# Kernel tuning notes

Measured on AMD Instinct MI355X. Metric: run time of the kernel, lower is better.

Reference implementation:

```python
import jax, jax.numpy as jnp
import numpy as np

B, M, N_CTR, K = 16, 2048, 512, 32
DIM, DEPTH, HEADS = 384, 6, 6
EMB = 48  # fourier embedding dim (48//6 = 8 freqs per axis, basis [3,24])


def make_basis():
    e = (2.0 ** np.arange(EMB // 6)).astype(np.float32) * np.pi  # [8]
    z = np.zeros(EMB // 6, np.float32)
    basis = np.stack([np.concatenate([e, z, z]),
                      np.concatenate([z, e, z]),
                      np.concatenate([z, z, e])])  # [3, 24]
    return jnp.asarray(basis)


def fourier_embed(x, basis):
    # x [..., 3] -> [..., 48]  (sin/cos of 24 frequency projections)
    p = jnp.einsum('...d,de->...e', x, basis)
    return jnp.concatenate([jnp.sin(p), jnp.cos(p)], axis=-1)


def fps_idx(pos, n):
    # farthest point sampling, deterministic start at index 0. pos [M,3] -> [n]
    d0 = jnp.sum((pos - pos[0]) ** 2, -1)
    def step(d, _):
        i = jnp.argmax(d)
        d = jnp.minimum(d, jnp.sum((pos - pos[i]) ** 2, -1))
        return d, i
    _, idxs = jax.lax.scan(step, d0, None, length=n - 1)
    return jnp.concatenate([jnp.zeros(1, jnp.int32), idxs.astype(jnp.int32)])


def layernorm(x, g, b, eps=1e-6):
    m = jnp.mean(x, -1, keepdims=True)
    v = jnp.var(x, -1, keepdims=True)
    return (x - m) * jax.lax.rsqrt(v + eps) * g + b


def _lin(key, fi, fo):
    kw, kb = jax.random.split(key)
    w = jax.random.normal(kw, (fi, fo), jnp.float32) / np.sqrt(fi)
    b = jax.random.normal(kb, (fo,), jnp.float32) * 0.01
    return w, b


def setup_inputs() -> dict:
    key = jax.random.key(0)
    ks = jax.random.split(key, 16)
    pc = jax.random.uniform(ks[0], (B, M, 3), jnp.float32)
    embed_w, embed_b = _lin(ks[1], 3 + EMB, DIM)
    lw1, lb1 = _lin(ks[2], 3 + EMB, 256)
    lw2, lb2 = _lin(ks[3], 256, 256)
    gw1, gb1 = _lin(ks[4], 256, 256)
    gw2, gb2 = _lin(ks[5], 256, DIM)
    def stack_lin(k, fi, fo):
        kk = jax.random.split(k, DEPTH)
        ws, bs = zip(*[_lin(kk[i], fi, fo) for i in range(DEPTH)])
        return jnp.stack(ws), jnp.stack(bs)
    qkv_w, qkv_b = stack_lin(ks[6], DIM, 3 * DIM)
    proj_w, proj_b = stack_lin(ks[7], DIM, DIM)
    fc1_w, fc1_b = stack_lin(ks[8], DIM, 4 * DIM)
    fc2_w, fc2_b = stack_lin(ks[9], 4 * DIM, DIM)
    return dict(
        pc=pc, embed_w=embed_w, embed_b=embed_b,
        lw1=lw1, lb1=lb1, lw2=lw2, lb2=lb2,
        gw1=gw1, gb1=gb1, gw2=gw2, gb2=gb2,
        ln1_g=jnp.ones((DEPTH, DIM)), ln1_b=jnp.zeros((DEPTH, DIM)),
        qkv_w=qkv_w, qkv_b=qkv_b, proj_w=proj_w, proj_b=proj_b,
        gamma1=jax.random.normal(ks[10], (DEPTH, DIM)) * 0.1,
        ln2_g=jnp.ones((DEPTH, DIM)), ln2_b=jnp.zeros((DEPTH, DIM)),
        fc1_w=fc1_w, fc1_b=fc1_b, fc2_w=fc2_w, fc2_b=fc2_b,
        gamma2=jax.random.normal(ks[11], (DEPTH, DIM)) * 0.1,
        lnf_g=jnp.ones((DIM,)), lnf_b=jnp.zeros((DIM,)),
    )


def reference(pc, embed_w, embed_b, lw1, lb1, lw2, lb2, gw1, gb1, gw2, gb2,
              ln1_g, ln1_b, qkv_w, qkv_b, proj_w, proj_b, gamma1,
              ln2_g, ln2_b, fc1_w, fc1_b, fc2_w, fc2_b, gamma2, lnf_g, lnf_b):
    basis = make_basis()
    # --- FPS centers (per batch) ---
    idx = jax.vmap(lambda p: fps_idx(p, N_CTR))(pc)                 # [B,N]
    centers = jnp.take_along_axis(pc, idx[:, :, None], axis=1)      # [B,N,3]
    # --- KNN graph: for each center, K nearest of the M points ---
    d2 = jnp.sum((centers[:, :, None, :] - pc[:, None, :, :]) ** 2, -1)  # [B,N,M]
    _, nn_idx = jax.lax.top_k(-d2, K)                               # [B,N,K]
    # --- PointConv: gather -> local MLP -> max-scatter -> global MLP ---
    src = jax.vmap(lambda p, i: p[i])(pc, nn_idx)                   # [B,N,K,3]
    rel = src - centers[:, :, None, :]
    feat = jnp.concatenate([rel, fourier_embed(rel, basis)], -1)    # [B,N,K,51]
    h = jax.nn.relu(feat @ lw1 + lb1) @ lw2 + lb2                   # [B,N,K,256]
    h = jnp.max(h, axis=2)  # scatter_max over edges == max over K neighbors
    x = jax.nn.relu(h @ gw1 + gb1) @ gw2 + gb2                      # [B,N,DIM]
    # --- positional embedding tokens ---
    pe = jnp.concatenate([centers, fourier_embed(centers, basis)], -1) @ embed_w + embed_b
    x = x + pe
    # --- ViT blocks (pre-LN, LayerScale, eval mode: no dropout/droppath) ---
    hd = DIM // HEADS
    scale = hd ** -0.5
    for l in range(DEPTH):
        xn = layernorm(x, ln1_g[l], ln1_b[l])
        qkv = (xn @ qkv_w[l] + qkv_b[l]).reshape(B, N_CTR, 3, HEADS, hd)
        q, k, v = jnp.moveaxis(qkv, 2, 0)                           # [B,N,H,hd]
        att = jax.nn.softmax(jnp.einsum('bqhd,bkhd->bhqk', q, k) * scale, axis=-1)
        o = jnp.einsum('bhqk,bkhd->bqhd', att, v).reshape(B, N_CTR, DIM)
        x = x + gamma1[l] * (o @ proj_w[l] + proj_b[l])
        xn = layernorm(x, ln2_g[l], ln2_b[l])
        mlp = jax.nn.gelu(xn @ fc1_w[l] + fc1_b[l], approximate=False) @ fc2_w[l] + fc2_b[l]
        x = x + gamma2[l] * mlp
    out = layernorm(x, lnf_g, lnf_b)
    return out, centers
```

## Files before the change

kernel.cpp:

```cpp
#include <hip/hip_runtime.h>
#include <math.h>

#define NB 16
#define NM 2048
#define NCTR 512
#define NK 32
#define NDIM 384

typedef unsigned long long ull;
typedef unsigned int uint;
typedef unsigned short ushort;
typedef __attribute__((ext_vector_type(8))) short bf16x8;
typedef __attribute__((ext_vector_type(4))) float f32x4;

__device__ __forceinline__ float dist2_exact(float ax, float ay, float az,
                                             float bx, float by, float bz) {
  float dx = __fsub_rn(ax, bx);
  float dy = __fsub_rn(ay, by);
  float dz = __fsub_rn(az, bz);
  return __fadd_rn(__fadd_rn(__fmul_rn(dx, dx), __fmul_rn(dy, dy)),
                   __fmul_rn(dz, dz));
}

__device__ __forceinline__ float gelu_f(float x) {
  return 0.5f * x * (1.0f + erff(x * 0.70710678118654752f));
}

__device__ __forceinline__ ushort f2bf(float f) {
  uint u = __float_as_uint(f);
  return (ushort)((u + 0x7FFFu + ((u >> 16) & 1u)) >> 16);
}
__device__ __forceinline__ float bf2f(ushort h) {
  return __uint_as_float(((uint)h) << 16);
}

__device__ __forceinline__ void cvt8(float4 p, float4 q, uint4& hi, uint4& lo) {
  float v0 = p.x, v1 = p.y, v2 = p.z, v3 = p.w;
  float v4 = q.x, v5 = q.y, v6 = q.z, v7 = q.w;
  ushort h0 = f2bf(v0), h1 = f2bf(v1), h2 = f2bf(v2), h3 = f2bf(v3);
  ushort h4 = f2bf(v4), h5 = f2bf(v5), h6 = f2bf(v6), h7 = f2bf(v7);
  ushort l0 = f2bf(v0 - bf2f(h0)), l1 = f2bf(v1 - bf2f(h1));
  ushort l2 = f2bf(v2 - bf2f(h2)), l3 = f2bf(v3 - bf2f(h3));
  ushort l4 = f2bf(v4 - bf2f(h4)), l5 = f2bf(v5 - bf2f(h5));
  ushort l6 = f2bf(v6 - bf2f(h6)), l7 = f2bf(v7 - bf2f(h7));
  hi.x = (uint)h0 | ((uint)h1 << 16); hi.y = (uint)h2 | ((uint)h3 << 16);
  hi.z = (uint)h4 | ((uint)h5 << 16); hi.w = (uint)h6 | ((uint)h7 << 16);
  lo.x = (uint)l0 | ((uint)l1 << 16); lo.y = (uint)l2 | ((uint)l3 << 16);
  lo.z = (uint)l4 | ((uint)l5 << 16); lo.w = (uint)l6 | ((uint)l7 << 16);
}

__device__ __forceinline__ void split_store(float v, ushort* H, ushort* L,
                                            size_t off) {
  ushort hi = f2bf(v);
  H[off] = hi;
  L[off] = f2bf(v - bf2f(hi));
}

__global__ __launch_bounds__(256)
void fps_kernel(const float* __restrict__ pc, float* __restrict__ centers) {
  int b = blockIdx.x;
  __shared__ float4 pos4[NM];
  __shared__ ull red[2][4];
  const float* pb = pc + (size_t)b * (NM * 3);
  int tid = threadIdx.x, lane = tid & 63, wv = tid >> 6;
  float px[8], py[8], pz[8];
#pragma unroll
  for (int i = 0; i < 8; ++i) {
    int p = tid + 256 * i;
    float x = pb[3 * p], y = pb[3 * p + 1], z = pb[3 * p + 2];
    px[i] = x; py[i] = y; pz[i] = z;
    pos4[p] = make_float4(x, y, z, 0.f);
  }
  __syncthreads();
  float* cb = centers + (size_t)b * (NCTR * 3);
  float4 s0 = pos4[0];
  float sx = s0.x, sy = s0.y, sz = s0.z;
  if (tid == 0) { cb[0] = sx; cb[1] = sy; cb[2] = sz; }
  float d[8];
  for (int n = 1; n < NCTR; ++n) {
    ull best = 0;
#pragma unroll
    for (int i = 0; i < 8; ++i) {
      int p = tid + 256 * i;
      float nd = dist2_exact(px[i], py[i], pz[i], sx, sy, sz);
      d[i] = (n == 1) ? nd : fminf(d[i], nd);
      ull key = ((ull)__float_as_uint(d[i]) << 32) | (unsigned)(0x7FFFFFFF - p);
      best = best > key ? best : key;
    }
#pragma unroll
    for (int off = 32; off; off >>= 1) {
      ull o = __shfl_xor(best, off);
      best = best > o ? best : o;
    }
    if (lane == 0) red[n & 1][wv] = best;
    __syncthreads();
    ull g0 = red[n & 1][0], g1 = red[n & 1][1];
    ull g2 = red[n & 1][2], g3 = red[n & 1][3];
    ull ga = g0 > g1 ? g0 : g1;
    ull gc2 = g2 > g3 ? g2 : g3;
    ull gb = ga > gc2 ? ga : gc2;
    int j = 0x7FFFFFFF - (int)(unsigned)(gb & 0xFFFFFFFFull);
    float4 np = pos4[j];
    sx = np.x; sy = np.y; sz = np.z;
    if (tid == 0) { cb[n * 3] = sx; cb[n * 3 + 1] = sy; cb[n * 3 + 2] = sz; }
  }
}

__global__ __launch_bounds__(256, 2)
void knn_kernel(const float* __restrict__ pc, const float* __restrict__ centers,
                int* __restrict__ nn) {
  __shared__ float pos[NM * 3];
  int b = blockIdx.x >> 7;
  int n0 = (blockIdx.x & 127) << 2;
  const float* pb = pc + (size_t)b * (NM * 3);
  for (int i = threadIdx.x; i < NM * 3; i += 256) pos[i] = pb[i];
  __syncthreads();
  int wv = threadIdx.x >> 6, lane = threadIdx.x & 63;
  int gc = b * NCTR + n0 + wv;
  float cx = centers[gc * 3], cy = centers[gc * 3 + 1], cz = centers[gc * 3 + 2];
  ull key[32];
  ull gmin[4];
#pragma unroll
  for (int g = 0; g < 4; ++g) {
    gmin[g] = ~0ull;
#pragma unroll
    for (int i = 0; i < 8; ++i) {
      int r = g * 8 + i;
      int p = lane + (r << 6);
      float nd = dist2_exact(pos[3 * p], pos[3 * p + 1], pos[3 * p + 2], cx, cy, cz);
      key[r] = ((ull)__float_as_uint(nd) << 11) | (unsigned)p;
      gmin[g] = gmin[g] < key[r] ? gmin[g] : key[r];
    }
  }
  ull a01 = gmin[0] < gmin[1] ? gmin[0] : gmin[1];
  ull a23 = gmin[2] < gmin[3] ? gmin[2] : gmin[3];
  ull lmin = a01 < a23 ? a01 : a23;
  int* nnc = nn + (size_t)gc * NK;
  for (int round = 0; round < NK; ++round) {
    ull w = lmin;
#pragma unroll
    for (int off = 32; off; off >>= 1) {
      ull o = __shfl_xor(w, off);
      w = w < o ? w : o;
    }
    if (lmin == w) {
      nnc[round] = (int)(w & 2047ull);
#pragma unroll
      for (int g = 0; g < 4; ++g) {
        if (gmin[g] == w) {
          gmin[g] = ~0ull;
#pragma unroll
          for (int i = 0; i < 8; ++i) {
            int r = g * 8 + i;
            key[r] = (key[r] == w) ? ~0ull : key[r];
            gmin[g] = gmin[g] < key[r] ? gmin[g] : key[r];
          }
        }
      }
      ull b01 = gmin[0] < gmin[1] ? gmin[0] : gmin[1];
      ull b23 = gmin[2] < gmin[3] ? gmin[2] : gmin[3];
      lmin = b01 < b23 ? b01 : b23;
    }
  }
}

__global__ __launch_bounds__(256)
void wconv(const float* __restrict__ W, ushort* __restrict__ out, int K8, int N,
           int Ksrc) {
  int c = blockIdx.x * 256 + threadIdx.x;
  if (c >= K8 * N) return;
  int kb = c / N, n = c - kb * N;
  float v[8];
#pragma unroll
  for (int i = 0; i < 8; ++i) {
    int row = kb * 8 + i;
    v[i] = (row < Ksrc) ? W[(size_t)row * N + n] : 0.f;
  }
  float4 p, q;
  p.x = v[0]; p.y = v[1]; p.z = v[2]; p.w = v[3];
  q.x = v[4]; q.y = v[5]; q.z = v[6]; q.w = v[7];
  uint4 hi, lo;
  cvt8(p, q, hi, lo);
  *(uint4*)(out + (size_t)c * 8) = hi;
  *(uint4*)(out + (size_t)(K8 * N + c) * 8) = lo;
}

__global__ __launch_bounds__(256, 2)
void edge_mfma(const float* __restrict__ pc, const float* __restrict__ centers,
               const int* __restrict__ nn, const ushort* __restrict__ lw1s,
               const float* __restrict__ lb1, const ushort* __restrict__ lw2s,
               const float* __restrict__ lb2, ushort* __restrict__ hH,
               ushort* __restrict__ hL) {
  __shared__ __align__(16) ushort featH[4096], featL[4096];
  __shared__ __align__(16) ushort t1H[16384], t1L[16384];
  int tid = threadIdx.x;
  int w = tid >> 6, lane = tid & 63;
  int l15 = lane & 15, l4 = lane >> 4;
  int wbase = w << 6;
  {
    int e = tid >> 2, s = tid & 3;
    int ge = blockIdx.x * 64 + e;
    int c = ge >> 5;
    int b = c >> 9;
    int j = nn[ge];
    const float* sp = pc + ((size_t)b * NM + j) * 3;
    float rx = sp[0] - centers[c * 3];
    float ry = sp[1] - centers[c * 3 + 1];
    float rz = sp[2] - centers[c * 3 + 2];
    auto putk = [&](int k, float v) {
      ushort hi = f2bf(v);
      ushort lo = f2bf(v - bf2f(hi));
      int idx = ((k >> 3) * 64 + e) * 8 + (k & 7);
      featH[idx] = hi;
      featL[idx] = lo;
    };
    if (s < 3) {
      float r = (s == 0) ? rx : (s == 1) ? ry : rz;
#pragma unroll
      for (int f = 0; f < 8; ++f) {
        float ef = (float)(M_PI * (double)(1 << f));
        float p = r * ef;
        putk(3 + 8 * s + f, sinf(p));
        putk(27 + 8 * s + f, cosf(p));
      }
    } else {
      putk(0, rx);
      putk(1, ry);
      putk(2, rz);
#pragma unroll
      for (int k = 51; k < 64; ++k) putk(k, 0.f);
    }
  }
  __syncthreads();
  const ushort* lw1H = lw1s;
  const ushort* lw1L = lw1s + 8 * 256 * 8;
  f32x4 acc1[4][4];
#pragma unroll
  for (int i = 0; i < 4; ++i)
#pragma unroll
    for (int j = 0; j < 4; ++j) acc1[i][j] = (f32x4){0.f, 0.f, 0.f, 0.f};
#pragma unroll
  for (int ks = 0; ks < 2; ++ks) {
    bf16x8 ah[4], al[4];
#pragma unroll
    for (int fm = 0; fm < 4; ++fm) {
      int idx = ((ks * 4 + l4) * 64 + fm * 16 + l15) * 8;
      ah[fm] = *(const bf16x8*)&featH[idx];
      al[fm] = *(const bf16x8*)&featL[idx];
    }
#pragma unroll
    for (int fn = 0; fn < 4; ++fn) {
      int col = wbase + fn * 16 + l15;
      size_t boff = ((size_t)(ks * 4 + l4) * 256 + col) * 8;
      bf16x8 bh = *(const bf16x8*)(lw1H + boff);
      bf16x8 bl = *(const bf16x8*)(lw1L + boff);
#pragma unroll
      for (int fm = 0; fm < 4; ++fm) {
        acc1[fm][fn] = __builtin_amdgcn_mfma_f32_16x16x32_bf16(al[fm], bh, acc1[fm][fn], 0, 0, 0);
        acc1[fm][fn] = __builtin_amdgcn_mfma_f32_16x16x32_bf16(ah[fm], bl, acc1[fm][fn], 0, 0, 0);
        acc1[fm][fn] = __builtin_amdgcn_mfma_f32_16x16x32_bf16(ah[fm], bh, acc1[fm][fn], 0, 0, 0);
      }
    }
  }
#pragma unroll
  for (int fn = 0; fn < 4; ++fn) {
    int chan = wbase + fn * 16 + l15;
    float bias = lb1[chan];
    int kb = chan >> 3, k7 = chan & 7;
#pragma unroll
    for (int fm = 0; fm < 4; ++fm) {
#pragma unroll
      for (int r = 0; r < 4; ++r) {
        int edge = fm * 16 + l4 * 4 + r;
        float v = fmaxf(acc1[fm][fn][r] + bias, 0.f);
        ushort hi = f2bf(v);
        ushort lo = f2bf(v - bf2f(hi));
        int idx = (kb * 64 + edge) * 8 + k7;
        t1H[idx] = hi;
        t1L[idx] = lo;
      }
    }
  }
  __syncthreads();
  const ushort* lw2H = lw2s;
  const ushort* lw2L = lw2s + 32 * 256 * 8;
  f32x4 acc2[4][4];
#pragma unroll
  for (int i = 0; i < 4; ++i)
#pragma unroll
    for (int j = 0; j < 4; ++j) acc2[i][j] = (f32x4){0.f, 0.f, 0.f, 0.f};
#pragma unroll
  for (int ks = 0; ks < 8; ++ks) {
    bf16x8 ah[4], al[4];
#pragma unroll
    for (int fm = 0; fm < 4; ++fm) {
      int idx = ((ks * 4 + l4) * 64 + fm * 16 + l15) * 8;
      ah[fm] = *(const bf16x8*)&t1H[idx];
      al[fm] = *(const bf16x8*)&t1L[idx];
    }
#pragma unroll
    for (int fn = 0; fn < 4; ++fn) {
      int col = wbase + fn * 16 + l15;
      size_t boff = ((size_t)(ks * 4 + l4) * 256 + col) * 8;
      bf16x8 bh = *(const bf16x8*)(lw2H + boff);
      bf16x8 bl = *(const bf16x8*)(lw2L + boff);
#pragma unroll
      for (int fm = 0; fm < 4; ++fm) {
        acc2[fm][fn] = __builtin_amdgcn_mfma_f32_16x16x32_bf16(al[fm], bh, acc2[fm][fn], 0, 0, 0);
        acc2[fm][fn] = __builtin_amdgcn_mfma_f32_16x16x32_bf16(ah[fm], bl, acc2[fm][fn], 0, 0, 0);
        acc2[fm][fn] = __builtin_amdgcn_mfma_f32_16x16x32_bf16(ah[fm], bh, acc2[fm][fn], 0, 0, 0);
      }
    }
  }
#pragma unroll
  for (int fn = 0; fn < 4; ++fn) {
    int col = wbase + fn * 16 + l15;
    float m0 = -INFINITY, m1 = -INFINITY;
#pragma unroll
    for (int r = 0; r < 4; ++r) {
      m0 = fmaxf(m0, fmaxf(acc2[0][fn][r], acc2[1][fn][r]));
      m1 = fmaxf(m1, fmaxf(acc2[2][fn][r], acc2[3][fn][r]));
    }
    m0 = fmaxf(m0, __shfl_xor(m0, 16));
    m0 = fmaxf(m0, __shfl_xor(m0, 32));
    m1 = fmaxf(m1, __shfl_xor(m1, 16));
    m1 = fmaxf(m1, __shfl_xor(m1, 32));
    if (l4 == 0) {
      float bias = lb2[col];
      int c0 = blockIdx.x * 2;
      split_store(m0 + bias, hH, hL, (size_t)c0 * 256 + col);
      split_store(m1 + bias, hH, hL, (size_t)(c0 + 1) * 256 + col);
    }
  }
}

template <int EPI, int OUTS>
__global__ __launch_bounds__(256, 2)
void gemm_s(const ushort* __restrict__ AH, const ushort* __restrict__ AL,
            const ushort* __restrict__ Wh, const ushort* __restrict__ Wl,
            const float* __restrict__ bias, const float* __restrict__ gamma,
            const float* __restrict__ resid, float* __restrict__ C,
            ushort* __restrict__ CH, ushort* __restrict__ CL,
            int M, int N, int K) {
  __shared__ __align__(16) ushort Ah[4096], Al[4096], Bh[4096], Bl[4096];
  int tid = threadIdx.x;
  int bn = blockIdx.x << 7, bm = blockIdx.y << 7;
  int wid = tid >> 6, lane = tid & 63;
  int wr = wid >> 1, wc = wid & 1;
  int l15 = lane & 15, l4 = lane >> 4;

  int arow = tid >> 1, akb0 = (tid & 1) << 1;
  const ushort* ApH = AH + (size_t)(bm + arow) * K + (akb0 << 3);
  const ushort* ApL = AL + (size_t)(bm + arow) * K + (akb0 << 3);
  int wkb = tid >> 7, wn = tid & 127;

  f32x4 acc[4][4];
#pragma unroll
  for (int i = 0; i < 4; ++i)
#pragma unroll
    for (int j = 0; j < 4; ++j) acc[i][j] = (f32x4){0.f, 0.f, 0.f, 0.f};

  uint4 a0 = *(const uint4*)(ApH + 0);
  uint4 a1 = *(const uint4*)(ApH + 8);
  uint4 a2 = *(const uint4*)(ApL + 0);
  uint4 a3 = *(const uint4*)(ApL + 8);
  size_t wo1 = ((size_t)wkb * N + bn + wn) * 8;
  size_t wo2 = ((size_t)(wkb + 2) * N + bn + wn) * 8;
  uint4 w0 = *(const uint4*)(Wh + wo1);
  uint4 w1 = *(const uint4*)(Wh + wo2);
  uint4 w2 = *(const uint4*)(Wl + wo1);
  uint4 w3 = *(const uint4*)(Wl + wo2);

  int nkt = K >> 5;
  for (int kt = 0; kt < nkt; ++kt) {
    *(uint4*)&Ah[(akb0 * 128 + arow) * 8] = a0;
    *(uint4*)&Ah[((akb0 + 1) * 128 + arow) * 8] = a1;
    *(uint4*)&Al[(akb0 * 128 + arow) * 8] = a2;
    *(uint4*)&Al[((akb0 + 1) * 128 + arow) * 8] = a3;
    *(uint4*)&Bh[tid * 8] = w0;
    *(uint4*)&Bh[(tid + 256) * 8] = w1;
    *(uint4*)&Bl[tid * 8] = w2;
    *(uint4*)&Bl[(tid + 256) * 8] = w3;
    __syncthreads();
    if (kt + 1 < nkt) {
      a0 = *(const uint4*)(ApH + (kt + 1) * 32 + 0);
      a1 = *(const uint4*)(ApH + (kt + 1) * 32 + 8);
      a2 = *(const uint4*)(ApL + (kt + 1) * 32 + 0);
      a3 = *(const uint4*)(ApL + (kt + 1) * 32 + 8);
      size_t b1 = ((size_t)((kt + 1) * 4 + wkb) * N + bn + wn) * 8;
      size_t b2 = ((size_t)((kt + 1) * 4 + wkb + 2) * N + bn + wn) * 8;
      w0 = *(const uint4*)(Wh + b1);
      w1 = *(const uint4*)(Wh + b2);
      w2 = *(const uint4*)(Wl + b1);
      w3 = *(const uint4*)(Wl + b2);
    }
    bf16x8 ahf[4], alf[4];
#pragma unroll
    for (int fm = 0; fm < 4; ++fm) {
      int ci = l4 * 128 + wr * 64 + fm * 16 + l15;
      ahf[fm] = *(bf16x8*)&Ah[ci * 8];
      alf[fm] = *(bf16x8*)&Al[ci * 8];
    }
#pragma unroll
    for (int fn = 0; fn < 4; ++fn) {
      int ci = l4 * 128 + wc * 64 + fn * 16 + l15;
      bf16x8 bh = *(bf16x8*)&Bh[ci * 8];
      bf16x8 bl = *(bf16x8*)&Bl[ci * 8];
#pragma unroll
      for (int fm = 0; fm < 4; ++fm) {
        acc[fm][fn] = __builtin_amdgcn_mfma_f32_16x16x32_bf16(alf[fm], bh, acc[fm][fn], 0, 0, 0);
        acc[fm][fn] = __builtin_amdgcn_mfma_f32_16x16x32_bf16(ahf[fm], bl, acc[fm][fn], 0, 0, 0);
        acc[fm][fn] = __builtin_amdgcn_mfma_f32_16x16x32_bf16(ahf[fm], bh, acc[fm][fn], 0, 0, 0);
      }
    }
    __syncthreads();
  }

#pragma unroll
  for (int fn = 0; fn < 4; ++fn) {
    int col = bn + wc * 64 + fn * 16 + l15;
    float bv = bias[col];
    float gv = (EPI == 3) ? gamma[col] : 0.f;
#pragma unroll
    for (int fm = 0; fm < 4; ++fm) {
      int row0 = bm + wr * 64 + fm * 16 + l4 * 4;
#pragma unroll
      for (int r = 0; r < 4; ++r) {
        float v = acc[fm][fn][r] + bv;
        if (EPI == 1) v = fmaxf(v, 0.f);
        else if (EPI == 2) v = gelu_f(v);
        else if (EPI == 3) v = resid[(size_t)(row0 + r) * N + col] + gv * v;
        size_t off = (size_t)(row0 + r) * N + col;
        if (OUTS == 0) C[off] = v;
        else split_store(v, CH, CL, off);
      }
    }
  }
}

__global__ __launch_bounds__(256)
void pe_add(const float* __restrict__ centers, const float* __restrict__ ew,
            const float* __restrict__ eb, float* x) {
  __shared__ float fc[51];
  int c = blockIdx.x, tid = threadIdx.x;
  if (tid < 24) {
    int a = tid >> 3, f = tid & 7;
    float coord = centers[c * 3 + a];
    float p = coord * (float)(M_PI * (double)(1 << f));
    fc[3 + tid] = sinf(p);
    fc[27 + tid] = cosf(p);
  } else if (tid < 27) {
    fc[tid - 24] = centers[c * 3 + (tid - 24)];
  }
  __syncthreads();
  for (int j = tid; j < NDIM; j += 256) {
    float acc = eb[j];
#pragma unroll
    for (int d = 0; d < 51; ++d) acc = fmaf(fc[d], ew[d * NDIM + j], acc);
    x[(size_t)c * NDIM + j] += acc;
  }
}

__global__ __launch_bounds__(256)
void ln_f32(const float* __restrict__ x, const float* __restrict__ g,
            const float* __restrict__ b, float* __restrict__ y) {
  int row = (blockIdx.x << 2) + (threadIdx.x >> 6);
  int lane = threadIdx.x & 63;
  const float* xr = x + (size_t)row * NDIM;
  float v[6];
#pragma unroll
  for (int i = 0; i < 6; ++i) v[i] = xr[lane + (i << 6)];
  float s = 0.f;
#pragma unroll
  for (int i = 0; i < 6; ++i) s += v[i];
#pragma unroll
  for (int off = 32; off; off >>= 1) s += __shfl_xor(s, off);
  float m = s / 384.f;
  float var = 0.f;
#pragma unroll
  for (int i = 0; i < 6; ++i) { float dd = v[i] - m; var += dd * dd; }
#pragma unroll
  for (int off = 32; off; off >>= 1) var += __shfl_xor(var, off);
  var = var / 384.f;
  float rs = 1.f / sqrtf(var + 1e-6f);
#pragma unroll
  for (int i = 0; i < 6; ++i) {
    int cc = lane + (i << 6);
    y[(size_t)row * NDIM + cc] = (v[i] - m) * rs * g[cc] + b[cc];
  }
}

__global__ __launch_bounds__(256)
void ln_split(const float* __restrict__ x, const float* __restrict__ g,
              const float* __restrict__ b, ushort* __restrict__ yH,
              ushort* __restrict__ yL) {
  int row = (blockIdx.x << 2) + (threadIdx.x >> 6);
  int lane = threadIdx.x & 63;
  const float* xr = x + (size_t)row * NDIM;
  float v[6];
#pragma unroll
  for (int i = 0; i < 6; ++i) v[i] = xr[lane + (i << 6)];
  float s = 0.f;
#pragma unroll
  for (int i = 0; i < 6; ++i) s += v[i];
#pragma unroll
  for (int off = 32; off; off >>= 1) s += __shfl_xor(s, off);
  float m = s / 384.f;
  float var = 0.f;
#pragma unroll
  for (int i = 0; i < 6; ++i) { float dd = v[i] - m; var += dd * dd; }
#pragma unroll
  for (int off = 32; off; off >>= 1) var += __shfl_xor(var, off);
  var = var / 384.f;
  float rs = 1.f / sqrtf(var + 1e-6f);
#pragma unroll
  for (int i = 0; i < 6; ++i) {
    int cc = lane + (i << 6);
    float yv = (v[i] - m) * rs * g[cc] + b[cc];
    split_store(yv, yH, yL, (size_t)row * NDIM + cc);
  }
}

__global__ __launch_bounds__(256, 2)
void attn_mfma(const ushort* __restrict__ FH, const ushort* __restrict__ FL,
               ushort* __restrict__ oH, ushort* __restrict__ oL) {
  __shared__ __align__(16) ushort kTH[4096], kTL[4096];
  __shared__ __align__(16) ushort vSH[4096], vSL[4096];
  __shared__ __align__(16) ushort pSH[8192], pSL[8192];
  int bi = blockIdx.x;
  int qt = bi & 3;
  int hh = (bi >> 2) % 6;
  int b = bi / 24;
  int tid = threadIdx.x;
  int w = tid >> 6, lane = tid & 63;
  int l15 = lane & 15, l4 = lane >> 4;
  const ushort* baseH = FH + (size_t)(b * NCTR) * 1152;
  const ushort* baseL = FL + (size_t)(b * NCTR) * 1152;
  int qbase = qt * 128 + w * 32;

  bf16x8 qh[2][2], ql[2][2];
#pragma unroll
  for (int qr = 0; qr < 2; ++qr) {
#pragma unroll
    for (int ds = 0; ds < 2; ++ds) {
      size_t off = (size_t)(qbase + qr * 16 + l15) * 1152 + hh * 64 + ds * 32 + l4 * 8;
      qh[qr][ds] = *(const bf16x8*)(baseH + off);
      ql[qr][ds] = *(const bf16x8*)(baseL + off);
    }
  }

  f32x4 oacc[2][4];
#pragma unroll
  for (int i = 0; i < 2; ++i)
#pragma unroll
    for (int j = 0; j < 4; ++j) oacc[i][j] = (f32x4){0.f, 0.f, 0.f, 0.f};
  float m_[2][4], l_[2][4];
#pragma unroll
  for (int i = 0; i < 2; ++i)
#pragma unroll
    for (int r = 0; r < 4; ++r) { m_[i][r] = -INFINITY; l_[i][r] = 0.f; }

  ushort* pHw = pSH + w * 2048;
  ushort* pLw = pSL + w * 2048;

  for (int ch = 0; ch < 8; ++ch) {
    {
      int key = tid & 63, dgh = tid >> 6;
      size_t krow = (size_t)(ch * 64 + key) * 1152 + 384 + hh * 64;
#pragma unroll
      for (int i = 0; i < 2; ++i) {
        int dg = dgh * 2 + i;
        *(uint4*)&kTH[(dg * 64 + key) * 8] = *(const uint4*)(baseH + krow + dg * 8);
        *(uint4*)&kTL[(dg * 64 + key) * 8] = *(const uint4*)(baseL + krow + dg * 8);
      }
      int d = tid & 63, kb2 = tid >> 6;
#pragma unroll
      for (int i = 0; i < 2; ++i) {
        int kb = kb2 + i * 4;
        ushort hv[8], lv[8];
#pragma unroll
        for (int j = 0; j < 8; ++j) {
          size_t off = (size_t)(ch * 64 + kb * 8 + j) * 1152 + 768 + hh * 64 + d;
          hv[j] = baseH[off];
          lv[j] = baseL[off];
        }
        uint4 H, L;
        H.x = (uint)hv[0] | ((uint)hv[1] << 16); H.y = (uint)hv[2] | ((uint)hv[3] << 16);
        H.z = (uint)hv[4] | ((uint)hv[5] << 16); H.w = (uint)hv[6] | ((uint)hv[7] << 16);
        L.x = (uint)lv[0] | ((uint)lv[1] << 16); L.y = (uint)lv[2] | ((uint)lv[3] << 16);
        L.z = (uint)lv[4] | ((uint)lv[5] << 16); L.w = (uint)lv[6] | ((uint)lv[7] << 16);
        *(uint4*)&vSH[(kb * 64 + d) * 8] = H;
        *(uint4*)&vSL[(kb * 64 + d) * 8] = L;
      }
    }
    __syncthreads();

    f32x4 sacc[2][4];
#pragma unroll
    for (int i = 0; i < 2; ++i)
#pragma unroll
      for (int j = 0; j < 4; ++j) sacc[i][j] = (f32x4){0.f, 0.f, 0.f, 0.f};
#pragma unroll
    for (int ds = 0; ds < 2; ++ds) {
#pragma unroll
      for (int kc = 0; kc < 4; ++kc) {
        int idx = ((ds * 4 + l4) * 64 + kc * 16 + l15) * 8;
        bf16x8 bh = *(const bf16x8*)&kTH[idx];
        bf16x8 bl = *(const bf16x8*)&kTL[idx];
#pragma unroll
        for (int qr = 0; qr < 2; ++qr) {
          sacc[qr][kc] = __builtin_amdgcn_mfma_f32_16x16x32_bf16(ql[qr][ds], bh, sacc[qr][kc], 0, 0, 0);
          sacc[qr][kc] = __builtin_amdgcn_mfma_f32_16x16x32_bf16(qh[qr][ds], bl, sacc[qr][kc], 0, 0, 0);
          sacc[qr][kc] = __builtin_amdgcn_mfma_f32_16x16x32_bf16(qh[qr][ds], bh, sacc[qr][kc], 0, 0, 0);
        }
      }
    }

    float t[2][4];
#pragma unroll
    for (int qr = 0; qr < 2; ++qr)
#pragma unroll
      for (int r = 0; r < 4; ++r) {
        float a0 = sacc[qr][0][r] * 0.125f; sacc[qr][0][r] = a0;
        float a1 = sacc[qr][1][r] * 0.125f; sacc[qr][1][r] = a1;
        float a2 = sacc[qr][2][r] * 0.125f; sacc[qr][2][r] = a2;
        float a3 = sacc[qr][3][r] * 0.125f; sacc[qr][3][r] = a3;
        t[qr][r] = fmaxf(fmaxf(a0, a1), fmaxf(a2, a3));
      }
#pragma unroll
    for (int off = 1; off < 16; off <<= 1)
#pragma unroll
      for (int qr = 0; qr < 2; ++qr)
#pragma unroll
        for (int r = 0; r < 4; ++r)
          t[qr][r] = fmaxf(t[qr][r], __shfl_xor(t[qr][r], off));
    float f_[2][4];
#pragma unroll
    for (int qr = 0; qr < 2; ++qr)
#pragma unroll
      for (int r = 0; r < 4; ++r) {
        float mn = fmaxf(m_[qr][r], t[qr][r]);
        f_[qr][r] = expf(m_[qr][r] - mn);
        m_[qr][r] = mn;
      }
#pragma unroll
    for (int qr = 0; qr < 2; ++qr)
#pragma unroll
      for (int dc = 0; dc < 4; ++dc)
#pragma unroll
        for (int r = 0; r < 4; ++r) oacc[qr][dc][r] *= f_[qr][r];
    float sm[2][4];
#pragma unroll
    for (int qr = 0; qr < 2; ++qr)
#pragma unroll
      for (int r = 0; r < 4; ++r) {
        float p0 = expf(sacc[qr][0][r] - m_[qr][r]); sacc[qr][0][r] = p0;
        float p1 = expf(sacc[qr][1][r] - m_[qr][r]); sacc[qr][1][r] = p1;
        float p2 = expf(sacc[qr][2][r] - m_[qr][r]); sacc[qr][2][r] = p2;
        float p3 = expf(sacc[qr][3][r] - m_[qr][r]); sacc[qr][3][r] = p3;
        sm[qr][r] = ((p0 + p1) + (p2 + p3));
      }
#pragma unroll
    for (int off = 1; off < 16; off <<= 1)
#pragma unroll
      for (int qr = 0; qr < 2; ++qr)
#pragma unroll
        for (int r = 0; r < 4; ++r)
          sm[qr][r] += __shfl_xor(sm[qr][r], off);
#pragma unroll
    for (int qr = 0; qr < 2; ++qr)
#pragma unroll
      for (int r = 0; r < 4; ++r) l_[qr][r] = l_[qr][r] * f_[qr][r] + sm[qr][r];

#pragma unroll
    for (int qr = 0; qr < 2; ++qr)
#pragma unroll
      for (int kc = 0; kc < 4; ++kc)
#pragma unroll
        for (int r = 0; r < 4; ++r) {
          float pv = sacc[qr][kc][r];
          ushort hi = f2bf(pv);
          ushort lo = f2bf(pv - bf2f(hi));
          int k = kc * 16 + l15;
          int qrow = qr * 16 + l4 * 4 + r;
          int idx = ((k >> 3) * 32 + qrow) * 8 + (k & 7);
          pHw[idx] = hi;
          pLw[idx] = lo;
        }

#pragma unroll
    for (int ks = 0; ks < 2; ++ks) {
      bf16x8 pah[2], pal[2];
#pragma unroll
      for (int qr = 0; qr < 2; ++qr) {
        int idx = ((ks * 4 + l4) * 32 + qr * 16 + l15) * 8;
        pah[qr] = *(const bf16x8*)&pHw[idx];
        pal[qr] = *(const bf16x8*)&pLw[idx];
      }
#pragma unroll
      for (int dc = 0; dc < 4; ++dc) {
        int idx = ((ks * 4 + l4) * 64 + dc * 16 + l15) * 8;
        bf16x8 vh = *(const bf16x8*)&vSH[idx];
        bf16x8 vl = *(const bf16x8*)&vSL[idx];
#pragma unroll
        for (int qr = 0; qr < 2; ++qr) {
          oacc[qr][dc] = __builtin_amdgcn_mfma_f32_16x16x32_bf16(pal[qr], vh, oacc[qr][dc], 0, 0, 0);
          oacc[qr][dc] = __builtin_amdgcn_mfma_f32_16x16x32_bf16(pah[qr], vl, oacc[qr][dc], 0, 0, 0);
          oacc[qr][dc] = __builtin_amdgcn_mfma_f32_16x16x32_bf16(pah[qr], vh, oacc[qr][dc], 0, 0, 0);
        }
      }
    }
    __syncthreads();
  }

  float il[2][4];
#pragma unroll
  for (int qr = 0; qr < 2; ++qr)
#pragma unroll
    for (int r = 0; r < 4; ++r) il[qr][r] = 1.f / l_[qr][r];
#pragma unroll
  for (int qr = 0; qr < 2; ++qr)
#pragma unroll
    for (int dc = 0; dc < 4; ++dc)
#pragma unroll
      for (int r = 0; r < 4; ++r) {
        int row = b * NCTR + qbase + qr * 16 + l4 * 4 + r;
        int col = hh * 64 + dc * 16 + l15;
        split_store(oacc[qr][dc][r] * il[qr][r], oH, oL, (size_t)row * NDIM + col);
      }
}

extern "C" void kernel_launch(void* const* d_in, const int* in_sizes, int n_in,
                              void* d_out, int out_size, void* d_ws, size_t ws_size,
                              hipStream_t stream) {
  const float* pc      = (const float*)d_in[0];
  const float* embed_w = (const float*)d_in[1];
  const float* embed_b = (const float*)d_in[2];
  const float* lw1     = (const float*)d_in[3];
  const float* lb1     = (const float*)d_in[4];
  const float* lw2     = (const float*)d_in[5];
  const float* lb2     = (const float*)d_in[6];
  const float* gw1     = (const float*)d_in[7];
  const float* gb1     = (const float*)d_in[8];
  const float* gw2     = (const float*)d_in[9];
  const float* gb2     = (const float*)d_in[10];
  const float* ln1_g   = (const float*)d_in[11];
  const float* ln1_b   = (const float*)d_in[12];
  const float* qkv_w   = (const float*)d_in[13];
  const float* qkv_b   = (const float*)d_in[14];
  const float* proj_w  = (const float*)d_in[15];
  const float* proj_b  = (const float*)d_in[16];
  const float* gamma1  = (const float*)d_in[17];
  const float* ln2_g   = (const float*)d_in[18];
  const float* ln2_b   = (const float*)d_in[19];
  const float* fc1_w   = (const float*)d_in[20];
  const float* fc1_b   = (const float*)d_in[21];
  const float* fc2_w   = (const float*)d_in[22];
  const float* fc2_b   = (const float*)d_in[23];
  const float* gamma2  = (const float*)d_in[24];
  const float* lnf_g   = (const float*)d_in[25];
  const float* lnf_b   = (const float*)d_in[26];

  float* out = (float*)d_out;
  float* centers = out + (size_t)NB * NCTR * NDIM;

  char* ws = (char*)d_ws;
  int*    nn  = (int*)(ws + 0);
  float*  x   = (float*)(ws + 1048576);
  ushort* xnH = (ushort*)(ws + 13631488);
  ushort* xnL = (ushort*)(ws + 19922944);
  ushort* FH  = (ushort*)(ws + 26214400);
  ushort* FL  = (ushort*)(ws + 51380224);
  ushort* hH  = (ushort*)(ws + 76546048);
  ushort* hL  = (ushort*)(ws + 80740352);
  ushort* wsplit = (ushort*)(ws + 84934656);

  size_t wofs = 0;
  auto convp = [&](const float* w, int Kpad, int N, int Ksrc) -> ushort* {
    ushort* dst = wsplit + wofs;
    int K8 = Kpad >> 3, total = K8 * N;
    wconv<<<(total + 255) / 256, 256, 0, stream>>>(w, dst, K8, N, Ksrc);
    wofs += (size_t)2 * Kpad * N;
    return dst;
  };
  ushort* qkvS = convp(qkv_w, 2304, 1152, 2304);
  ushort* projS = convp(proj_w, 2304, 384, 2304);
  ushort* fc1S = convp(fc1_w, 2304, 1536, 2304);
  ushort* fc2S = convp(fc2_w, 9216, 384, 9216);
  ushort* g1S  = convp(gw1, 256, 256, 256);
  ushort* g2S  = convp(gw2, 256, 384, 256);
  ushort* lw1s = convp(lw1, 64, 256, 51);
  ushort* lw2s = convp(lw2, 256, 256, 256);

  fps_kernel<<<NB, 256, 0, stream>>>(pc, centers);
  knn_kernel<<<2048, 256, 0, stream>>>(pc, centers, nn);
  edge_mfma<<<4096, 256, 0, stream>>>(pc, centers, nn, lw1s, lb1, lw2s, lb2, hH, hL);

  gemm_s<1, 1><<<dim3(2, 64), 256, 0, stream>>>(hH, hL, g1S, g1S + 65536, gb1,
                                                nullptr, nullptr, nullptr, xnH, xnL,
                                                8192, 256, 256);
  gemm_s<0, 0><<<dim3(3, 64), 256, 0, stream>>>(xnH, xnL, g2S, g2S + 98304, gb2,
                                                nullptr, nullptr, x, nullptr, nullptr,
                                                8192, 384, 256);
  pe_add<<<8192, 256, 0, stream>>>(centers, embed_w, embed_b, x);

  for (int l = 0; l < 6; ++l) {
    ln_split<<<2048, 256, 0, stream>>>(x, ln1_g + l * 384, ln1_b + l * 384, xnH, xnL);
    gemm_s<0, 1><<<dim3(9, 64), 256, 0, stream>>>(
        xnH, xnL, qkvS + (size_t)l * 442368, qkvS + 2654208 + (size_t)l * 442368,
        qkv_b + l * 1152, nullptr, nullptr, nullptr, FH, FL, 8192, 1152, 384);
    attn_mfma<<<384, 256, 0, stream>>>(FH, FL, xnH, xnL);
    gemm_s<3, 0><<<dim3(3, 64), 256, 0, stream>>>(
        xnH, xnL, projS + (size_t)l * 147456, projS + 884736 + (size_t)l * 147456,
        proj_b + l * 384, gamma1 + l * 384, x, x, nullptr, nullptr, 8192, 384, 384);
    ln_split<<<2048, 256, 0, stream>>>(x, ln2_g + l * 384, ln2_b + l * 384, xnH, xnL);
    gemm_s<2, 1><<<dim3(12, 64), 256, 0, stream>>>(
        xnH, xnL, fc1S + (size_t)l * 589824, fc1S + 3538944 + (size_t)l * 589824,
        fc1_b + l * 1536, nullptr, nullptr, nullptr, FH, FL, 8192, 1536, 384);
    gemm_s<3, 0><<<dim3(3, 64), 256, 0, stream>>>(
        FH, FL, fc2S + (size_t)l * 589824, fc2S + 3538944 + (size_t)l * 589824,
        fc2_b + l * 384, gamma2 + l * 384, x, x, nullptr, nullptr, 8192, 384, 1536);
  }
  ln_f32<<<2048, 256, 0, stream>>>(x, lnf_g, lnf_b, out);
}
```

Before: 2.026 ms.

## Use direct global-to-LDS loads in GEMM, add BM=64 tiles, fast FPS argmax

After: 2.145 ms. 5.9% more time.

```diff
diff --git a/kernel.cpp b/kernel.cpp
--- a/kernel.cpp
+++ b/kernel.cpp
@@ -56,6 +56,12 @@
   L[off] = f2bf(v - bf2f(hi));
 }
 
+__device__ __forceinline__ void gload16(const ushort* g, ushort* l) {
+  __builtin_amdgcn_global_load_lds(
+      (const __attribute__((address_space(1))) void*)g,
+      (__attribute__((address_space(3))) void*)l, 16, 0, 0);
+}
+
 __global__ __launch_bounds__(256)
 void fps_kernel(const float* __restrict__ pc, float* __restrict__ centers) {
   int b = blockIdx.x;
@@ -87,12 +93,24 @@
       ull key = ((ull)__float_as_uint(d[i]) << 32) | (unsigned)(0x7FFFFFFF - p);
       best = best > key ? best : key;
     }
-#pragma unroll
-    for (int off = 32; off; off >>= 1) {
-      ull o = __shfl_xor(best, off);
-      best = best > o ? best : o;
-    }
-    if (lane == 0) red[n & 1][wv] = best;
+    float dl = __uint_as_float((uint)(best >> 32));
+    float wm = dl;
+#pragma unroll
+    for (int off = 32; off; off >>= 1) wm = fmaxf(wm, __shfl_xor(wm, off));
+    ull mask = __ballot(dl == wm);
+    ull wkey;
+    if (mask & (mask - 1)) {
+      wkey = best;
+#pragma unroll
+      for (int off = 32; off; off >>= 1) {
+        ull o = __shfl_xor(wkey, off);
+        wkey = wkey > o ? wkey : o;
+      }
+    } else {
+      int src = __ffsll((long long)mask) - 1;
+      wkey = __shfl(best, src);
+    }
+    if (lane == 0) red[n & 1][wv] = wkey;
     __syncthreads();
     ull g0 = red[n & 1][0], g1 = red[n & 1][1];
     ull g2 = red[n & 1][2], g3 = red[n & 1][3];
@@ -334,7 +352,7 @@
   }
 }
 
-template <int EPI, int OUTS>
+template <int EPI, int OUTS, int BM>
 __global__ __launch_bounds__(256, 2)
 void gemm_s(const ushort* __restrict__ AH, const ushort* __restrict__ AL,
             const ushort* __restrict__ Wh, const ushort* __restrict__ Wl,
@@ -342,68 +360,53 @@
             const float* __restrict__ resid, float* __restrict__ C,
             ushort* __restrict__ CH, ushort* __restrict__ CL,
             int M, int N, int K) {
-  __shared__ __align__(16) ushort Ah[4096], Al[4096], Bh[4096], Bl[4096];
+  constexpr int WC = (BM == 128) ? 2 : 4;
+  constexpr int FN = 128 / (WC * 16);
+  constexpr int ACH = BM / 64;
+  __shared__ __align__(16) ushort Ah[BM * 32], Al[BM * 32];
+  __shared__ __align__(16) ushort Bh[4096], Bl[4096];
   int tid = threadIdx.x;
-  int bn = blockIdx.x << 7, bm = blockIdx.y << 7;
+  int bn = blockIdx.x << 7, bm = blockIdx.y * BM;
   int wid = tid >> 6, lane = tid & 63;
-  int wr = wid >> 1, wc = wid & 1;
+  int wr = (BM == 128) ? (wid >> 1) : 0;
+  int wc = (BM == 128) ? (wid & 1) : wid;
   int l15 = lane & 15, l4 = lane >> 4;
 
-  int arow = tid >> 1, akb0 = (tid & 1) << 1;
-  const ushort* ApH = AH + (size_t)(bm + arow) * K + (akb0 << 3);
-  const ushort* ApL = AL + (size_t)(bm + arow) * K + (akb0 << 3);
-  int wkb = tid >> 7, wn = tid & 127;
-
-  f32x4 acc[4][4];
+  f32x4 acc[4][FN];
 #pragma unroll
   for (int i = 0; i < 4; ++i)
 #pragma unroll
-    for (int j = 0; j < 4; ++j) acc[i][j] = (f32x4){0.f, 0.f, 0.f, 0.f};
-
-  uint4 a0 = *(const uint4*)(ApH + 0);
-  uint4 a1 = *(const uint4*)(ApH + 8);
-  uint4 a2 = *(const uint4*)(ApL + 0);
-  uint4 a3 = *(const uint4*)(ApL + 8);
-  size_t wo1 = ((size_t)wkb * N + bn + wn) * 8;
-  size_t wo2 = ((size_t)(wkb + 2) * N + bn + wn) * 8;
-  uint4 w0 = *(const uint4*)(Wh + wo1);
-  uint4 w1 = *(const uint4*)(Wh + wo2);
-  uint4 w2 = *(const uint4*)(Wl + wo1);
-  uint4 w3 = *(const uint4*)(Wl + wo2);
+    for (int j = 0; j < FN; ++j) acc[i][j] = (f32x4){0.f, 0.f, 0.f, 0.f};
 
   int nkt = K >> 5;
   for (int kt = 0; kt < nkt; ++kt) {
-    *(uint4*)&Ah[(akb0 * 128 + arow) * 8] = a0;
-    *(uint4*)&Ah[((akb0 + 1) * 128 + arow) * 8] = a1;
-    *(uint4*)&Al[(akb0 * 128 + arow) * 8] = a2;
-    *(uint4*)&Al[((akb0 + 1) * 128 + arow) * 8] = a3;
-    *(uint4*)&Bh[tid * 8] = w0;
-    *(uint4*)&Bh[(tid + 256) * 8] = w1;
-    *(uint4*)&Bl[tid * 8] = w2;
-    *(uint4*)&Bl[(tid + 256) * 8] = w3;
+#pragma unroll
+    for (int q = 0; q < ACH; ++q) {
+      int e = q * 256 + tid;
+      int kb = e / BM, row = e % BM;
+      size_t so = (size_t)(bm + row) * K + kt * 32 + kb * 8;
+      gload16(AH + so, &Ah[e * 8]);
+      gload16(AL + so, &Al[e * 8]);
+    }
+#pragma unroll
+    for (int q = 0; q < 2; ++q) {
+      int e = q * 256 + tid;
+      int kb = e >> 7, n = e & 127;
+      size_t so = ((size_t)(kt * 4 + kb) * N + bn + n) * 8;
+      gload16(Wh + so, &Bh[e * 8]);
+      gload16(Wl + so, &Bl[e * 8]);
+    }
     __syncthreads();
-    if (kt + 1 < nkt) {
-      a0 = *(const uint4*)(ApH + (kt + 1) * 32 + 0);
-      a1 = *(const uint4*)(ApH + (kt + 1) * 32 + 8);
-      a2 = *(const uint4*)(ApL + (kt + 1) * 32 + 0);
-      a3 = *(const uint4*)(ApL + (kt + 1) * 32 + 8);
-      size_t b1 = ((size_t)((kt + 1) * 4 + wkb) * N + bn + wn) * 8;
-      size_t b2 = ((size_t)((kt + 1) * 4 + wkb + 2) * N + bn + wn) * 8;
-      w0 = *(const uint4*)(Wh + b1);
-      w1 = *(const uint4*)(Wh + b2);
-      w2 = *(const uint4*)(Wl + b1);
-      w3 = *(const uint4*)(Wl + b2);
-    }
     bf16x8 ahf[4], alf[4];
 #pragma unroll
     for (int fm = 0; fm < 4; ++fm) {
-      int ci = l4 * 128 + wr * 64 + fm * 16 + l15;
+      int ci = l4 * BM + wr * 64 + fm * 16 + l15;
       ahf[fm] = *(bf16x8*)&Ah[ci * 8];
       alf[fm] = *(bf16x8*)&Al[ci * 8];
     }
 #pragma unroll
-    for (int fn = 0; fn < 4; ++fn) {
-      int ci = l4 * 128 + wc * 64 + fn * 16 + l15;
+    for (int fn = 0; fn < FN; ++fn) {
+      int ci = l4 * 128 + wc * (FN * 16) + fn * 16 + l15;
       bf16x8 bh = *(bf16x8*)&Bh[ci * 8];
       bf16x8 bl = *(bf16x8*)&Bl[ci * 8];
 #pragma unroll
@@ -417,8 +420,8 @@
   }
 
 #pragma unroll
-  for (int fn = 0; fn < 4; ++fn) {
-    int col = bn + wc * 64 + fn * 16 + l15;
+  for (int fn = 0; fn < FN; ++fn) {
+    int col = bn + wc * (FN * 16) + fn * 16 + l15;
     float bv = bias[col];
     float gv = (EPI == 3) ? gamma[col] : 0.f;
 #pragma unroll
@@ -796,28 +799,28 @@
   knn_kernel<<<2048, 256, 0, stream>>>(pc, centers, nn);
   edge_mfma<<<4096, 256, 0, stream>>>(pc, centers, nn, lw1s, lb1, lw2s, lb2, hH, hL);
 
-  gemm_s<1, 1><<<dim3(2, 64), 256, 0, stream>>>(hH, hL, g1S, g1S + 65536, gb1,
-                                                nullptr, nullptr, nullptr, xnH, xnL,
-                                                8192, 256, 256);
-  gemm_s<0, 0><<<dim3(3, 64), 256, 0, stream>>>(xnH, xnL, g2S, g2S + 98304, gb2,
-                                                nullptr, nullptr, x, nullptr, nullptr,
-                                                8192, 384, 256);
+  gemm_s<1, 1, 64><<<dim3(2, 128), 256, 0, stream>>>(
+      hH, hL, g1S, g1S + 65536, gb1, nullptr, nullptr, nullptr, xnH, xnL,
+      8192, 256, 256);
+  gemm_s<0, 0, 64><<<dim3(3, 128), 256, 0, stream>>>(
+      xnH, xnL, g2S, g2S + 98304, gb2, nullptr, nullptr, x, nullptr, nullptr,
+      8192, 384, 256);
   pe_add<<<8192, 256, 0, stream>>>(centers, embed_w, embed_b, x);
 
   for (int l = 0; l < 6; ++l) {
     ln_split<<<2048, 256, 0, stream>>>(x, ln1_g + l * 384, ln1_b + l * 384, xnH, xnL);
-    gemm_s<0, 1><<<dim3(9, 64), 256, 0, stream>>>(
+    gemm_s<0, 1, 128><<<dim3(9, 64), 256, 0, stream>>>(
         xnH, xnL, qkvS + (size_t)l * 442368, qkvS + 2654208 + (size_t)l * 442368,
         qkv_b + l * 1152, nullptr, nullptr, nullptr, FH, FL, 8192, 1152, 384);
     attn_mfma<<<384, 256, 0, stream>>>(FH, FL, xnH, xnL);
-    gemm_s<3, 0><<<dim3(3, 64), 256, 0, stream>>>(
+    gemm_s<3, 0, 64><<<dim3(3, 128), 256, 0, stream>>>(
         xnH, xnL, projS + (size_t)l * 147456, projS + 884736 + (size_t)l * 147456,
         proj_b + l * 384, gamma1 + l * 384, x, x, nullptr, nullptr, 8192, 384, 384);
     ln_split<<<2048, 256, 0, stream>>>(x, ln2_g + l * 384, ln2_b + l * 384, xnH, xnL);
-    gemm_s<2, 1><<<dim3(12, 64), 256, 0, stream>>>(
+    gemm_s<2, 1, 128><<<dim3(12, 64), 256, 0, stream>>>(
         xnH, xnL, fc1S + (size_t)l * 589824, fc1S + 3538944 + (size_t)l * 589824,
         fc1_b + l * 1536, nullptr, nullptr, nullptr, FH, FL, 8192, 1536, 384);
-    gemm_s<3, 0><<<dim3(3, 64), 256, 0, stream>>>(
+    gemm_s<3, 0, 64><<<dim3(3, 128), 256, 0, stream>>>(
         FH, FL, fc2S + (size_t)l * 589824, fc2S + 3538944 + (size_t)l * 589824,
         fc2_b + l * 384, gamma2 + l * 384, x, x, nullptr, nullptr, 8192, 384, 1536);
   }
```
